# Kernel optimization log

Hardware: AMD Instinct MI355X
Metric: run time of the kernel (lower is better)

Reference implementation:

```python
import jax, jax.numpy as jnp
import numpy as np
from jax import lax

H_STEP = 1.0 / 3.0  # h = (t1 - t0) / N with t0=0, t1=1, N=3
N_STEPS = 3


def _conv(x, w):
    # x: [B, C, H, W], w: [O, I, kh, kw], 'same' padding, stride 1
    return lax.conv_general_dilated(
        x, w, window_strides=(1, 1), padding='SAME',
        dimension_numbers=('NCHW', 'OIHW', 'NCHW'))


def setup_inputs() -> dict:
    key = jax.random.key(0)
    ks = jax.random.split(key, 5)
    B, C, H, W = 16, 128, 128, 128
    fan_in = C * 9
    return {
        'x': jax.random.normal(ks[0], (B, C, H, W), dtype=jnp.float32),
        'w1': jax.random.normal(ks[1], (C, C, 3, 3), dtype=jnp.float32) * (2.0 / fan_in) ** 0.5,
        'b1': jax.random.normal(ks[2], (C,), dtype=jnp.float32) * 0.01,
        'w2': jax.random.normal(ks[3], (C, C, 3, 3), dtype=jnp.float32) * (2.0 / fan_in) ** 0.5,
        'b2': jax.random.normal(ks[4], (C,), dtype=jnp.float32) * 0.01,
    }


def reference(x, w1, b1, w2, b2):
    # Euler-step residual block: x <- x + h * conv2(relu(conv1(x))) for N steps
    for _ in range(N_STEPS):
        t = jax.nn.relu(_conv(x, w1) + b1[None, :, None, None])
        x = x + H_STEP * (_conv(t, w2) + b2[None, :, None, None])
    return jax.nn.relu(x)
```

## Files before the change

### kernel.cpp

```cpp
#include <hip/hip_runtime.h>
#include <hip/hip_bf16.h>


#define BATCH 16
#define CH    128
#define HH    128
#define WW    128
#define H_STEP (1.0f/3.0f)

typedef short bf16x8 __attribute__((ext_vector_type(8)));
typedef float f32x4  __attribute__((ext_vector_type(4)));

__device__ __forceinline__ float bf2f(unsigned short u) {
    union { unsigned int i; float f; } c; c.i = ((unsigned int)u) << 16; return c.f;
}
__device__ __forceinline__ unsigned short f2bf(float f) {
    union { float f; unsigned int i; } c; c.f = f;
    unsigned int i = c.i;
    return (unsigned short)((i + 0x7FFFu + ((i >> 16) & 1u)) >> 16);
}

__device__ __forceinline__ void gload16(const unsigned short* g, unsigned short* l) {
    __builtin_amdgcn_global_load_lds(
        (const __attribute__((address_space(1))) unsigned int*)g,
        (__attribute__((address_space(3))) unsigned int*)l, 16, 0, 0);
}

__global__ __launch_bounds__(256)
void transpose_x(const float* __restrict__ x, unsigned short* __restrict__ xb)
{
    __shared__ unsigned short s[128 * 132];
    const int tid = threadIdx.x;
    const int bz  = blockIdx.x;
    const int b = bz >> 7, y = bz & 127;

    #pragma unroll
    for (int it = 0; it < 16; ++it) {
        int idx = it * 256 + tid;
        int ci = idx >> 5, xq = idx & 31;
        float4 v = *(const float4*)&x[(((size_t)b * CH + ci) * HH + y) * WW + xq * 4];
        uint2 p;
        p.x = (unsigned int)f2bf(v.x) | ((unsigned int)f2bf(v.y) << 16);
        p.y = (unsigned int)f2bf(v.z) | ((unsigned int)f2bf(v.w) << 16);
        *(uint2*)&s[ci * 132 + xq * 4] = p;
    }
    __syncthreads();
    #pragma unroll
    for (int it = 0; it < 8; ++it) {
        int idx = it * 256 + tid;
        int xx = idx >> 4, cc = idx & 15;
        unsigned short t[8];
        #pragma unroll
        for (int k = 0; k < 8; ++k) t[k] = s[(cc * 8 + k) * 132 + xx];
        uint4 p;
        p.x = (unsigned int)t[0] | ((unsigned int)t[1] << 16);
        p.y = (unsigned int)t[2] | ((unsigned int)t[3] << 16);
        p.z = (unsigned int)t[4] | ((unsigned int)t[5] << 16);
        p.w = (unsigned int)t[6] | ((unsigned int)t[7] << 16);
        *(uint4*)&xb[((size_t)(b * HH + y) * WW + xx) * CH + cc * 8] = p;
    }
}

__global__ __launch_bounds__(256)
void convert_w(const float* __restrict__ w, unsigned short* __restrict__ wb)
{
    int idx = blockIdx.x * 256 + threadIdx.x;
    #pragma unroll
    for (int t = 0; t < 9; ++t)
        wb[t * 16384 + idx] = f2bf(w[(size_t)idx * 9 + t]);
}

template<int MODE>
__global__ __launch_bounds__(128, 2)
void conv_mfma(const unsigned short* __restrict__ in,
               const unsigned short* __restrict__ wb,
               const float* __restrict__ bias,
               const unsigned short* resb,
               unsigned short* outb,
               float* __restrict__ outf)
{
    __shared__ __align__(16) char smem[41216];
    unsigned short* s_is = (unsigned short*)smem;
    unsigned short* s_w  = (unsigned short*)(smem + 16640);

    const int tid = threadIdx.x;
    const int bz0 = blockIdx.x;
    const int bz  = ((bz0 & 7) << 8) | (bz0 >> 3);
    const int b = bz >> 7, y = bz & 127;

    const int lane = tid & 63;
    const int wid  = tid >> 6;
    const int n16  = lane & 15;
    const int q    = lane >> 4;

    const int srow = lane >> 2;
    const int slot = lane & 3;

    const int kylo = (y == 0)      ? 1 : 0;
    const int kyhi = (y == HH - 1) ? 1 : 2;
    const int nky  = kyhi - kylo + 1;
    const int NG   = nky * 4;
    const int NS   = NG * 3;

    f32x4 acc[4][8];
    #pragma unroll
    for (int i = 0; i < 4; ++i)
        #pragma unroll
        for (int j = 0; j < 8; ++j) acc[i][j] = (f32x4)0.0f;

    auto stage_w = [&](int tap, int kq, int buf) {
        const unsigned short* wt = wb + tap * 16384 + kq * 32;
        #pragma unroll
        for (int c = 0; c < 4; ++c) {
            int row = (wid * 4 + c) * 16 + srow;
            const unsigned short* src = wt + row * 128 + ((slot ^ (row & 3)) << 3);
            gload16(src, s_w + buf * 4096 + (wid * 4 + c) * 512);
        }
    };
    auto stage_is = [&](int gy, int kq, int buf) {
        const size_t inrow = ((size_t)(b * HH + gy) * WW) * CH + kq * 32;
        #pragma unroll
        for (int c = 0; c < 4; ++c) {
            int r   = (wid * 4 + c) * 16 + srow;
            int swz = (r + 1) & 3;
            const unsigned short* src = in + inrow + (size_t)r * CH + ((slot ^ swz) << 3);
            gload16(src, s_is + buf * 4160 + ((wid * 4 + c) * 16 + 1) * 32);
        }
    };

    stage_w(kylo * 3 + 0, 0, 0);
    stage_is(y + kylo - 1, 0, 0);
    stage_w(kylo * 3 + 1, 0, 1);
    if (tid < 16) {
        int bfi = tid >> 3, rr = ((tid >> 2) & 1) ? 129 : 0, cc = tid & 3;
        uint4 z = {0u, 0u, 0u, 0u};
        *(uint4*)&s_is[bfi * 4160 + rr * 32 + cc * 8] = z;
    }
    asm volatile("s_waitcnt lgkmcnt(0)" ::: "memory");

    const int NSm1 = NS - 1;
    for (int s = 0; s < NS; ++s) {
        const int g   = s / 3;
        const int kx  = s - g * 3;
        const int ig  = g & 1;

        if (kx == 0) asm volatile("s_waitcnt vmcnt(4)" ::: "memory");
        else         asm volatile("s_waitcnt vmcnt(8)" ::: "memory");
        asm volatile("s_barrier" ::: "memory");

        {
            int wb2 = (kx == 0) ? 2 : (kx - 1);
            int s2  = s + 2; if (s2 > NSm1) s2 = NSm1;
            int g2  = s2 / 3, kx2 = s2 - g2 * 3;
            stage_w((kylo + (g2 >> 2)) * 3 + kx2, g2 & 3, wb2);
        }
        if (kx == 0) {
            int gn = g + 1; if (gn > NG - 1) gn = NG - 1;
            stage_is(y + kylo + (gn >> 2) - 1, gn & 3, (g + 1) & 1);
        }

        bf16x8 af[4], bfr[8];
        #pragma unroll
        for (int i = 0; i < 4; ++i) {
            int row = wid * 64 + i * 16 + n16;
            af[i] = *(const bf16x8*)&s_w[kx * 4096 + row * 32 + ((q ^ (row & 3)) << 3)];
        }
        #pragma unroll
        for (int j = 0; j < 8; ++j) {
            int rowb = j * 16 + n16 + kx;
            bfr[j] = *(const bf16x8*)&s_is[ig * 4160 + rowb * 32 + ((q ^ (rowb & 3)) << 3)];
        }
        __builtin_amdgcn_s_setprio(1);
        #pragma unroll
        for (int i = 0; i < 4; ++i)
            #pragma unroll
            for (int j = 0; j < 8; ++j)
                acc[i][j] = __builtin_amdgcn_mfma_f32_16x16x32_bf16(
                    af[i], bfr[j], acc[i][j], 0, 0, 0);
        __builtin_amdgcn_s_setprio(0);
    }

    const int ybase = (b * HH + y) * WW;
    if (MODE == 0) {
        asm volatile("s_waitcnt vmcnt(0) lgkmcnt(0)" ::: "memory");
        asm volatile("s_barrier" ::: "memory");
        unsigned short* sep = (unsigned short*)smem;
        #pragma unroll
        for (int j = 0; j < 8; ++j) {
            int px = j * 16 + n16;
            int sw = (px & 7) << 5;
            #pragma unroll
            for (int i = 0; i < 4; ++i) {
                int oc0 = wid * 64 + i * 16 + q * 4;
                float v0 = fmaxf(acc[i][j][0] + bias[oc0 + 0], 0.f);
                float v1 = fmaxf(acc[i][j][1] + bias[oc0 + 1], 0.f);
                float v2 = fmaxf(acc[i][j][2] + bias[oc0 + 2], 0.f);
                float v3 = fmaxf(acc[i][j][3] + bias[oc0 + 3], 0.f);
                uint2 po;
                po.x = (unsigned int)f2bf(v0) | ((unsigned int)f2bf(v1) << 16);
                po.y = (unsigned int)f2bf(v2) | ((unsigned int)f2bf(v3) << 16);
                *(uint2*)((char*)sep + ((px * 256 + oc0 * 2) ^ sw)) = po;
            }
        }
        asm volatile("s_waitcnt lgkmcnt(0)" ::: "memory");
        asm volatile("s_barrier" ::: "memory");
        #pragma unroll
        for (int it = 0; it < 16; ++it) {
            int idx = it * 128 + tid;
            int pxr = idx >> 4, cc = idx & 15;
            uint4 v = *(uint4*)((char*)sep + ((pxr * 256 + cc * 16) ^ ((pxr & 7) << 5)));
            *(uint4*)&outb[(size_t)(ybase + pxr) * CH + cc * 8] = v;
        }
    } else if (MODE == 1) {
        asm volatile("s_waitcnt vmcnt(0) lgkmcnt(0)" ::: "memory");
        asm volatile("s_barrier" ::: "memory");
        float* sf = (float*)smem;
        #pragma unroll
        for (int p = 0; p < 2; ++p) {
            if (p) {
                asm volatile("s_waitcnt lgkmcnt(0)" ::: "memory");
                asm volatile("s_barrier" ::: "memory");
            }
            #pragma unroll
            for (int jj = 0; jj < 4; ++jj) {
                int j   = p * 4 + jj;
                int pxl = jj * 16 + n16;
                int sw  = (pxl & 7) << 5;
                #pragma unroll
                for (int i = 0; i < 4; ++i) {
                    int oc0 = wid * 64 + i * 16 + q * 4;
                    f32x4 w = acc[i][j];
                    w[0] += bias[oc0 + 0]; w[1] += bias[oc0 + 1];
                    w[2] += bias[oc0 + 2]; w[3] += bias[oc0 + 3];
                    *(f32x4*)((char*)sf + ((pxl * 512 + oc0 * 4) ^ sw)) = w;
                }
            }
            asm volatile("s_waitcnt lgkmcnt(0)" ::: "memory");
            asm volatile("s_barrier" ::: "memory");
            #pragma unroll
            for (int it = 0; it < 16; ++it) {
                int idx = it * 128 + tid;
                int pxl = idx >> 5, c4 = idx & 31;
                f32x4 v = *(f32x4*)((char*)sf +
                            ((pxl * 512 + c4 * 16) ^ ((pxl & 7) << 5)));
                size_t gb = (size_t)(ybase + p * 64 + pxl) * CH + c4 * 4;
                uint2 rr = *(const uint2*)&resb[gb];
                float o0 = bf2f((unsigned short)(rr.x & 0xffff)) + H_STEP * v[0];
                float o1 = bf2f((unsigned short)(rr.x >> 16))    + H_STEP * v[1];
                float o2 = bf2f((unsigned short)(rr.y & 0xffff)) + H_STEP * v[2];
                float o3 = bf2f((unsigned short)(rr.y >> 16))    + H_STEP * v[3];
                uint2 po;
                po.x = (unsigned int)f2bf(o0) | ((unsigned int)f2bf(o1) << 16);
                po.y = (unsigned int)f2bf(o2) | ((unsigned int)f2bf(o3) << 16);
                *(uint2*)&outb[gb] = po;
            }
        }
    } else {
        #pragma unroll
        for (int i = 0; i < 4; ++i) {
            #pragma unroll
            for (int r = 0; r < 4; ++r) {
                int oc = wid * 64 + i * 16 + q * 4 + r;
                float bv = bias[oc];
                size_t orow = ((size_t)(b * CH + oc) * HH + y) * WW;
                #pragma unroll
                for (int j = 0; j < 8; ++j) {
                    int x = j * 16 + n16;
                    float v = acc[i][j][r] + bv;
                    v = bf2f(resb[(size_t)(ybase + x) * CH + oc]) + H_STEP * v;
                    outf[orow + x] = fmaxf(v, 0.f);
                }
            }
        }
    }
}

extern "C" void kernel_launch(void* const* d_in, const int* in_sizes, int n_in,
                              void* d_out, int out_size, void* d_ws, size_t ws_size,
                              hipStream_t stream) {
    const float* x0 = (const float*)d_in[0];
    const float* w1 = (const float*)d_in[1];
    const float* b1 = (const float*)d_in[2];
    const float* w2 = (const float*)d_in[3];
    const float* b2 = (const float*)d_in[4];

    const size_t NELEM = (size_t)BATCH * CH * HH * WW;
    unsigned short* XB = (unsigned short*)d_ws;
    unsigned short* T  = XB + NELEM;

    unsigned short* WB1;
    if (ws_size >= NELEM * 4 + 2 * 294912)
        WB1 = T + NELEM;
    else
        WB1 = (unsigned short*)d_in[0];
    unsigned short* WB2 = WB1 + 9 * 16384;

    dim3 block(256);
    dim3 block2(128);
    dim3 gridRow(BATCH * HH);

    transpose_x<<<gridRow, block, 0, stream>>>(x0, XB);
    convert_w<<<dim3(64), block, 0, stream>>>(w1, WB1);
    convert_w<<<dim3(64), block, 0, stream>>>(w2, WB2);

    conv_mfma<0><<<gridRow, block2, 0, stream>>>(XB, WB1, b1, nullptr, T, nullptr);
    conv_mfma<1><<<gridRow, block2, 0, stream>>>(T, WB2, b2, XB, XB, nullptr);
    conv_mfma<0><<<gridRow, block2, 0, stream>>>(XB, WB1, b1, nullptr, T, nullptr);
    conv_mfma<1><<<gridRow, block2, 0, stream>>>(T, WB2, b2, XB, XB, nullptr);
    conv_mfma<0><<<gridRow, block2, 0, stream>>>(XB, WB1, b1, nullptr, T, nullptr);
    conv_mfma<2><<<gridRow, block2, 0, stream>>>(T, WB2, b2, XB, nullptr, (float*)d_out);
}
```

Before: 875.1 us.

## Process two output rows per 256-thread block sharing staged weight tiles

Each conv block now has four waves and covers two image rows (y and y+64), so every weight tile staged into shared memory serves both rows. This halves weight traffic into LDS per output. Border rows are no longer handled by trimming the ky loop; they read from a zeroed LDS region, so the loop always runs 36 steps. Shared memory grows to about 66KB per block, which may limit occupancy, and boundary rows now do some wasted MFMA work.

```diff
diff --git a/kernel.cpp b/kernel.cpp
--- a/kernel.cpp
+++ b/kernel.cpp
@@ -71,7 +71,7 @@
 }
 
 template<int MODE>
-__global__ __launch_bounds__(128, 2)
+__global__ __launch_bounds__(256, 2)
 void conv_mfma(const unsigned short* __restrict__ in,
                const unsigned short* __restrict__ wb,
                const float* __restrict__ bias,
@@ -79,29 +79,28 @@
                unsigned short* outb,
                float* __restrict__ outf)
 {
-    __shared__ __align__(16) char smem[41216];
-    unsigned short* s_is = (unsigned short*)smem;
-    unsigned short* s_w  = (unsigned short*)(smem + 16640);
+    __shared__ __align__(16) char smem[66176];
+    unsigned short* s_is   = (unsigned short*)smem;
+    unsigned short* s_zero = (unsigned short*)smem + 16640;
+    unsigned short* s_w    = (unsigned short*)smem + 20800;
 
     const int tid = threadIdx.x;
     const int bz0 = blockIdx.x;
-    const int bz  = ((bz0 & 7) << 8) | (bz0 >> 3);
-    const int b = bz >> 7, y = bz & 127;
+    const int bz  = ((bz0 & 7) << 7) | (bz0 >> 3);
+    const int b  = bz >> 6, yp = bz & 63;
+    const int yA = yp, yB = yp + 64;
 
     const int lane = tid & 63;
     const int wid  = tid >> 6;
+    const int win  = wid & 1;
+    const int och  = (wid >> 1) * 64;
+    const int yw   = win ? yB : yA;
     const int n16  = lane & 15;
     const int q    = lane >> 4;
 
     const int srow = lane >> 2;
     const int slot = lane & 3;
 
-    const int kylo = (y == 0)      ? 1 : 0;
-    const int kyhi = (y == HH - 1) ? 1 : 2;
-    const int nky  = kyhi - kylo + 1;
-    const int NG   = nky * 4;
-    const int NS   = NG * 3;
-
     f32x4 acc[4][8];
     #pragma unroll
     for (int i = 0; i < 4; ++i)
@@ -111,64 +110,82 @@
     auto stage_w = [&](int tap, int kq, int buf) {
         const unsigned short* wt = wb + tap * 16384 + kq * 32;
         #pragma unroll
-        for (int c = 0; c < 4; ++c) {
-            int row = (wid * 4 + c) * 16 + srow;
-            const unsigned short* src = wt + row * 128 + ((slot ^ (row & 3)) << 3);
-            gload16(src, s_w + buf * 4096 + (wid * 4 + c) * 512);
+        for (int c = 0; c < 2; ++c) {
+            int row = (wid * 2 + c) * 16 + srow;
+            const unsigned short* src = wt + row * 128 + ((slot ^ ((row >> 1) & 3)) << 3);
+            gload16(src, s_w + buf * 4096 + (wid * 2 + c) * 512);
         }
     };
-    auto stage_is = [&](int gy, int kq, int buf) {
+    auto stage_is = [&](int gy, int kq, int sl) {
+        gy = gy < 0 ? 0 : (gy > HH - 1 ? HH - 1 : gy);
         const size_t inrow = ((size_t)(b * HH + gy) * WW) * CH + kq * 32;
         #pragma unroll
-        for (int c = 0; c < 4; ++c) {
-            int r   = (wid * 4 + c) * 16 + srow;
-            int swz = (r + 1) & 3;
-            const unsigned short* src = in + inrow + (size_t)r * CH + ((slot ^ swz) << 3);
-            gload16(src, s_is + buf * 4160 + ((wid * 4 + c) * 16 + 1) * 32);
+        for (int c = 0; c < 2; ++c) {
+            int r = (wid * 2 + c) * 16 + srow;
+            const unsigned short* src =
+                in + inrow + (size_t)r * CH + ((slot ^ (((r + 1) >> 1) & 3)) << 3);
+            gload16(src, s_is + sl * 4160 + ((wid * 2 + c) * 16 + 1) * 32);
         }
     };
 
-    stage_w(kylo * 3 + 0, 0, 0);
-    stage_is(y + kylo - 1, 0, 0);
-    stage_w(kylo * 3 + 1, 0, 1);
-    if (tid < 16) {
-        int bfi = tid >> 3, rr = ((tid >> 2) & 1) ? 129 : 0, cc = tid & 3;
+    stage_w(0, 0, 0);
+    stage_is(yA - 1, 0, 0);
+    stage_is(yB - 1, 0, 2);
+    stage_w(1, 0, 1);
+    #pragma unroll
+    for (int it = 0; it < 3; ++it) {
+        int idx = it * 256 + tid;
+        if (idx < 520) {
+            uint4 z = {0u, 0u, 0u, 0u};
+            *(uint4*)&s_zero[idx * 8] = z;
+        }
+    }
+    if (tid < 32) {
+        int sl = tid >> 3, hr = ((tid >> 2) & 1) ? 129 : 0, cc = tid & 3;
         uint4 z = {0u, 0u, 0u, 0u};
-        *(uint4*)&s_is[bfi * 4160 + rr * 32 + cc * 8] = z;
+        *(uint4*)&s_is[sl * 4160 + hr * 32 + cc * 8] = z;
     }
     asm volatile("s_waitcnt lgkmcnt(0)" ::: "memory");
 
-    const int NSm1 = NS - 1;
-    for (int s = 0; s < NS; ++s) {
-        const int g   = s / 3;
-        const int kx  = s - g * 3;
-        const int ig  = g & 1;
-
-        if (kx == 0) asm volatile("s_waitcnt vmcnt(4)" ::: "memory");
-        else         asm volatile("s_waitcnt vmcnt(8)" ::: "memory");
+    int kx = 0, g = 0;
+    for (int s = 0; s < 36; ++s) {
+        const int ky = g >> 2;
+        const int ib = g & 1;
+
+        if (kx == 0) asm volatile("s_waitcnt vmcnt(2)" ::: "memory");
+        else         asm volatile("s_waitcnt vmcnt(6)" ::: "memory");
         asm volatile("s_barrier" ::: "memory");
 
         {
+            int g2 = g, kx2 = kx + 2;
+            if (kx2 >= 3) { kx2 -= 3; ++g2; }
+            if (g2 > 11)  { g2 = 11; kx2 = 2; }
             int wb2 = (kx == 0) ? 2 : (kx - 1);
-            int s2  = s + 2; if (s2 > NSm1) s2 = NSm1;
-            int g2  = s2 / 3, kx2 = s2 - g2 * 3;
-            stage_w((kylo + (g2 >> 2)) * 3 + kx2, g2 & 3, wb2);
+            stage_w((g2 >> 2) * 3 + kx2, g2 & 3, wb2);
         }
         if (kx == 0) {
-            int gn = g + 1; if (gn > NG - 1) gn = NG - 1;
-            stage_is(y + kylo + (gn >> 2) - 1, gn & 3, (g + 1) & 1);
-        }
+            int gn = g + 1; if (gn > 11) gn = 11;
+            int kyn = gn >> 2, kqn = gn & 3, bn = gn & 1;
+            stage_is(yA + kyn - 1, kqn, bn);
+            stage_is(yB + kyn - 1, kqn, 2 + bn);
+        }
+
+        const int gyw = yw + ky - 1;
+        const unsigned short* ibase =
+            (gyw >= 0 && gyw < HH) ? (s_is + (win * 2 + ib) * 4160) : s_zero;
 
         bf16x8 af[4], bfr[8];
         #pragma unroll
         for (int i = 0; i < 4; ++i) {
-            int row = wid * 64 + i * 16 + n16;
-            af[i] = *(const bf16x8*)&s_w[kx * 4096 + row * 32 + ((q ^ (row & 3)) << 3)];
+            int row = och + i * 16 + n16;
+            af[i] = *(const bf16x8*)&s_w[kx * 4096 + row * 32 +
+                                         ((q ^ ((row >> 1) & 3)) << 3)];
         }
         #pragma unroll
         for (int j = 0; j < 8; ++j) {
             int rowb = j * 16 + n16 + kx;
-            bfr[j] = *(const bf16x8*)&s_is[ig * 4160 + rowb * 32 + ((q ^ (rowb & 3)) << 3)];
+            bfr[j] = *(const bf16x8*)&ibase[rowb * 32 +
+                                           ((q ^ ((rowb >> 1) & 3)) << 3)];
         }
         __builtin_amdgcn_s_setprio(1);
         #pragma unroll
@@ -178,12 +195,15 @@
                 acc[i][j] = __builtin_amdgcn_mfma_f32_16x16x32_bf16(
                     af[i], bfr[j], acc[i][j], 0, 0, 0);
         __builtin_amdgcn_s_setprio(0);
-    }
-
-    const int ybase = (b * HH + y) * WW;
+
+        if (++kx == 3) { kx = 0; ++g; }
+    }
+
+    asm volatile("s_waitcnt vmcnt(0) lgkmcnt(0)" ::: "memory");
+    asm volatile("s_barrier" ::: "memory");
+    const size_t ybw = (size_t)(b * HH + yw) * WW;
+
     if (MODE == 0) {
-        asm volatile("s_waitcnt vmcnt(0) lgkmcnt(0)" ::: "memory");
-        asm volatile("s_barrier" ::: "memory");
         unsigned short* sep = (unsigned short*)smem;
         #pragma unroll
         for (int j = 0; j < 8; ++j) {
@@ -191,7 +211,7 @@
             int sw = (px & 7) << 5;
             #pragma unroll
             for (int i = 0; i < 4; ++i) {
-                int oc0 = wid * 64 + i * 16 + q * 4;
+                int oc0 = och + i * 16 + q * 4;
                 float v0 = fmaxf(acc[i][j][0] + bias[oc0 + 0], 0.f);
                 float v1 = fmaxf(acc[i][j][1] + bias[oc0 + 1], 0.f);
                 float v2 = fmaxf(acc[i][j][2] + bias[oc0 + 2], 0.f);
@@ -199,28 +219,25 @@
                 uint2 po;
                 po.x = (unsigned int)f2bf(v0) | ((unsigned int)f2bf(v1) << 16);
                 po.y = (unsigned int)f2bf(v2) | ((unsigned int)f2bf(v3) << 16);
-                *(uint2*)((char*)sep + ((px * 256 + oc0 * 2) ^ sw)) = po;
+                *(uint2*)((char*)sep + win * 32768 + ((px * 256 + oc0 * 2) ^ sw)) = po;
             }
         }
         asm volatile("s_waitcnt lgkmcnt(0)" ::: "memory");
         asm volatile("s_barrier" ::: "memory");
         #pragma unroll
         for (int it = 0; it < 16; ++it) {
-            int idx = it * 128 + tid;
-            int pxr = idx >> 4, cc = idx & 15;
-            uint4 v = *(uint4*)((char*)sep + ((pxr * 256 + cc * 16) ^ ((pxr & 7) << 5)));
-            *(uint4*)&outb[(size_t)(ybase + pxr) * CH + cc * 8] = v;
+            int idx = it * 256 + tid;
+            int w2 = idx >> 11, pxr = (idx >> 4) & 127, cc = idx & 15;
+            uint4 v = *(uint4*)((char*)smem + w2 * 32768 +
+                                ((pxr * 256 + cc * 16) ^ ((pxr & 7) << 5)));
+            int y2 = w2 ? yB : yA;
+            *(uint4*)&outb[((size_t)(b * HH + y2) * WW + pxr) * CH + cc * 8] = v;
         }
     } else if (MODE == 1) {
-        asm volatile("s_waitcnt vmcnt(0) lgkmcnt(0)" ::: "memory");
-        asm volatile("s_barrier" ::: "memory");
         float* sf = (float*)smem;
         #pragma unroll
         for (int p = 0; p < 2; ++p) {
-            if (p) {
-                asm volatile("s_waitcnt lgkmcnt(0)" ::: "memory");
-                asm volatile("s_barrier" ::: "memory");
-            }
+            if (p) asm volatile("s_barrier" ::: "memory");
             #pragma unroll
             for (int jj = 0; jj < 4; ++jj) {
                 int j   = p * 4 + jj;
@@ -228,22 +245,23 @@
                 int sw  = (pxl & 7) << 5;
                 #pragma unroll
                 for (int i = 0; i < 4; ++i) {
-                    int oc0 = wid * 64 + i * 16 + q * 4;
+                    int oc0 = och + i * 16 + q * 4;
                     f32x4 w = acc[i][j];
                     w[0] += bias[oc0 + 0]; w[1] += bias[oc0 + 1];
                     w[2] += bias[oc0 + 2]; w[3] += bias[oc0 + 3];
-                    *(f32x4*)((char*)sf + ((pxl * 512 + oc0 * 4) ^ sw)) = w;
+                    *(f32x4*)((char*)sf + win * 32768 + ((pxl * 512 + oc0 * 4) ^ sw)) = w;
                 }
             }
             asm volatile("s_waitcnt lgkmcnt(0)" ::: "memory");
             asm volatile("s_barrier" ::: "memory");
             #pragma unroll
             for (int it = 0; it < 16; ++it) {
-                int idx = it * 128 + tid;
-                int pxl = idx >> 5, c4 = idx & 31;
-                f32x4 v = *(f32x4*)((char*)sf +
-                            ((pxl * 512 + c4 * 16) ^ ((pxl & 7) << 5)));
-                size_t gb = (size_t)(ybase + p * 64 + pxl) * CH + c4 * 4;
+                int idx = it * 256 + tid;
+                int w2 = idx >> 11, pxl = (idx >> 5) & 63, c4 = idx & 31;
+                f32x4 v = *(f32x4*)((char*)sf + w2 * 32768 +
+                                    ((pxl * 512 + c4 * 16) ^ ((pxl & 7) << 5)));
+                int y2 = w2 ? yB : yA;
+                size_t gb = ((size_t)(b * HH + y2) * WW + p * 64 + pxl) * CH + c4 * 4;
                 uint2 rr = *(const uint2*)&resb[gb];
                 float o0 = bf2f((unsigned short)(rr.x & 0xffff)) + H_STEP * v[0];
                 float o1 = bf2f((unsigned short)(rr.x >> 16))    + H_STEP * v[1];
@@ -260,14 +278,14 @@
         for (int i = 0; i < 4; ++i) {
             #pragma unroll
             for (int r = 0; r < 4; ++r) {
-                int oc = wid * 64 + i * 16 + q * 4 + r;
+                int oc = och + i * 16 + q * 4 + r;
                 float bv = bias[oc];
-                size_t orow = ((size_t)(b * CH + oc) * HH + y) * WW;
+                size_t orow = ((size_t)(b * CH + oc) * HH + yw) * WW;
                 #pragma unroll
                 for (int j = 0; j < 8; ++j) {
                     int x = j * 16 + n16;
                     float v = acc[i][j][r] + bv;
-                    v = bf2f(resb[(size_t)(ybase + x) * CH + oc]) + H_STEP * v;
+                    v = bf2f(resb[(ybw + x) * CH + oc]) + H_STEP * v;
                     outf[orow + x] = fmaxf(v, 0.f);
                 }
             }
@@ -296,17 +314,17 @@
     unsigned short* WB2 = WB1 + 9 * 16384;
 
     dim3 block(256);
-    dim3 block2(128);
     dim3 gridRow(BATCH * HH);
+    dim3 gridConv(BATCH * 64);
 
     transpose_x<<<gridRow, block, 0, stream>>>(x0, XB);
     convert_w<<<dim3(64), block, 0, stream>>>(w1, WB1);
     convert_w<<<dim3(64), block, 0, stream>>>(w2, WB2);
 
-    conv_mfma<0><<<gridRow, block2, 0, stream>>>(XB, WB1, b1, nullptr, T, nullptr);
-    conv_mfma<1><<<gridRow, block2, 0, stream>>>(T, WB2, b2, XB, XB, nullptr);
-    conv_mfma<0><<<gridRow, block2, 0, stream>>>(XB, WB1, b1, nullptr, T, nullptr);
-    conv_mfma<1><<<gridRow, block2, 0, stream>>>(T, WB2, b2, XB, XB, nullptr);
-    conv_mfma<0><<<gridRow, block2, 0, stream>>>(XB, WB1, b1, nullptr, T, nullptr);
-    conv_mfma<2><<<gridRow, block2, 0, stream>>>(T, WB2, b2, XB, nullptr, (float*)d_out);
-}
+    conv_mfma<0><<<gridConv, block, 0, stream>>>(XB, WB1, b1, nullptr, T, nullptr);
+    conv_mfma<1><<<gridConv, block, 0, stream>>>(T, WB2, b2, XB, XB, nullptr);
+    conv_mfma<0><<<gridConv, block, 0, stream>>>(XB, WB1, b1, nullptr, T, nullptr);
+    conv_mfma<1><<<gridConv, block, 0, stream>>>(T, WB2, b2, XB, XB, nullptr);
+    conv_mfma<0><<<gridConv, block, 0, stream>>>(XB, WB1, b1, nullptr, T, nullptr);
+    conv_mfma<2><<<gridConv, block, 0, stream>>>(T, WB2, b2, XB, nullptr, (float*)d_out);
+}
```

Measured after the change: 717.1 us. 18.1% less time.
